# Kernel optimization log

Measured on AMD Instinct MI355X. Metric: run time of the kernel, lower is better.

Reference implementation:

```python
import jax, jax.numpy as jnp
import numpy as np

N = 50000
E = 800000
C_IN = 64
C_OUT = 64
K = 3  # Chebyshev order (num_stacks)
LAMBDA_MAX = 2.0


def setup_inputs() -> dict:
    key = jax.random.key(0)
    ks = jax.random.split(key, 32)
    inp = {
        'X': jax.random.normal(ks[0], (N, C_IN), dtype=jnp.float32),
        'edge_index': jax.random.randint(ks[1], (2, E), 0, N, dtype=jnp.int64),
        'edge_weight': jax.random.uniform(ks[2], (E,), dtype=jnp.float32),
        'H': jax.random.normal(ks[3], (N, C_OUT), dtype=jnp.float32),
        'C': jax.random.normal(ks[4], (N, C_OUT), dtype=jnp.float32),
    }
    # 8 ChebConvs: conv_{x,h}_{i,f,c,o}; x-convs map C_IN->C_OUT, h-convs C_OUT->C_OUT
    names_x = ['Wxi', 'Wxf', 'Wxc', 'Wxo']
    names_h = ['Whi', 'Whf', 'Whc', 'Who']
    i = 5
    for nx, nh in zip(names_x, names_h):
        inp[nx] = jax.random.normal(ks[i], (K, C_IN, C_OUT), dtype=jnp.float32) * (1.0 / np.sqrt(K * C_IN)); i += 1
        inp['b' + nx[1:]] = jax.random.normal(ks[i], (C_OUT,), dtype=jnp.float32) * 0.01; i += 1
        inp[nh] = jax.random.normal(ks[i], (K, C_OUT, C_OUT), dtype=jnp.float32) * (1.0 / np.sqrt(K * C_OUT)); i += 1
        inp['b' + nh[1:]] = jax.random.normal(ks[i], (C_OUT,), dtype=jnp.float32) * 0.01; i += 1
    # per-gate biases b_i, b_f, b_c, b_o of shape [1, C_OUT] (zero-initialized in torch)
    for nm in ['bi', 'bf', 'bc', 'bo']:
        inp[nm] = jax.random.normal(ks[i], (1, C_OUT), dtype=jnp.float32) * 0.01; i += 1
    return inp


def _cheb_norm(edge_index, edge_weight, n):
    # symmetric normalization: D^-1/2 W D^-1/2 (PyG get_laplacian 'sym')
    row, col = edge_index[0], edge_index[1]
    deg = jax.ops.segment_sum(edge_weight, row, num_segments=n)
    dinv = jnp.where(deg > 0, jax.lax.rsqrt(jnp.where(deg > 0, deg, 1.0)), 0.0)
    return dinv[row] * edge_weight * dinv[col]


def _cheb_conv(x, W, b, row, col, nw, n):
    # ChebConv: out = sum_k T_k(L_hat) x @ W[k] + b, with
    # L_hat v = (2/lambda_max) * (v - A_norm v) - v
    def Lhat(v):
        agg = jax.ops.segment_sum(nw[:, None] * v[col], row, num_segments=n)
        return (2.0 / LAMBDA_MAX) * (v - agg) - v
    Tx_prev = x
    out = x @ W[0]
    k = W.shape[0]
    if k > 1:
        Tx = Lhat(x)
        out = out + Tx @ W[1]
        for j in range(2, k):
            Tx_new = 2.0 * Lhat(Tx) - Tx_prev
            out = out + Tx_new @ W[j]
            Tx_prev, Tx = Tx, Tx_new
    return out + b


def reference(X, edge_index, edge_weight, H, C,
              Wxi, bxi, Whi, bhi, Wxf, bxf, Whf, bhf,
              Wxc, bxc, Whc, bhc, Wxo, bxo, Who, bho,
              bi, bf, bc, bo):
    n = X.shape[0]
    row, col = edge_index[0], edge_index[1]
    nw = _cheb_norm(edge_index, edge_weight, n)
    cc = lambda v, W, b: _cheb_conv(v, W, b, row, col, nw, n)
    I = jax.nn.sigmoid(cc(X, Wxi, bxi) + cc(H, Whi, bhi) + bi)
    F = jax.nn.sigmoid(cc(X, Wxf, bxf) + cc(H, Whf, bhf) + bf)
    T = jnp.tanh(cc(X, Wxc, bxc) + cc(H, Whc, bhc) + bc)
    C_new = F * C + I * T
    O = jax.nn.sigmoid(cc(X, Wxo, bxo) + cc(H, Who, bho) + bo)
    H_new = O * jnp.tanh(C_new)
    return (H_new, C_new)
```

## Files before the change

### kernel.cpp

```cpp
#include <hip/hip_runtime.h>

#define N_NODES 50000
#define N_PAD   50048
#define N_EDGES 800000
#define NBE4    782
#define NB_IL2  1563

typedef __attribute__((ext_vector_type(8))) short bf16x8;
typedef __attribute__((ext_vector_type(4))) float f32x4;

__device__ __forceinline__ unsigned short f2bf(float f) {
    unsigned u = __float_as_uint(f);
    u = (u + 0x7fffu + ((u >> 16) & 1u)) >> 16;
    return (unsigned short)u;
}

__device__ __forceinline__ float fsig(float x) {
    x = fminf(fmaxf(x, -30.f), 30.f);
    float t = __expf(x);
    return __fdividef(t, 1.f + t);
}
__device__ __forceinline__ float ftanh(float x) {
    x = fminf(fmaxf(x, -15.f), 15.f);
    float t = __expf(2.f * x);
    return 1.f - __fdividef(2.f, t + 1.f);
}


__global__ __launch_bounds__(256) void k_deg_prep(
    const void* __restrict__ eiraw, const float* __restrict__ w,
    unsigned* __restrict__ packed, unsigned* __restrict__ rank,
    const float* __restrict__ X, const float* __restrict__ H, unsigned short* __restrict__ XH,
    const float* __restrict__ Wxi, const float* __restrict__ Whi,
    const float* __restrict__ Wxf, const float* __restrict__ Whf,
    const float* __restrict__ Wxc, const float* __restrict__ Whc,
    const float* __restrict__ Wxo, const float* __restrict__ Who,
    const float* __restrict__ bxi, const float* __restrict__ bhi,
    const float* __restrict__ bxf, const float* __restrict__ bhf,
    const float* __restrict__ bxc, const float* __restrict__ bhc,
    const float* __restrict__ bxo, const float* __restrict__ bho,
    const float* __restrict__ bgi, const float* __restrict__ bgf,
    const float* __restrict__ bgc, const float* __restrict__ bgo,
    unsigned short* __restrict__ Wf, float* __restrict__ ball) {
    __shared__ int sflag;
    int b = blockIdx.x, t = threadIdx.x;
    if (b < NBE4) {
        if (t == 0) sflag = 0;
        __syncthreads();
        int si = b * 1024 + t;
        int sv = ((const int*)eiraw)[1 + 2 * si];
        if (sv) atomicOr(&sflag, 1);
        __syncthreads();
        int is32 = sflag;

        int rr[4]; unsigned qq[4]; int ee[4];
#pragma unroll
        for (int k = 0; k < 4; k++) {
            int e = b * 1024 + k * 256 + t;
            ee[k] = e;
            if (e < N_EDGES) {
                rr[k] = is32 ? ((const int*)eiraw)[e] : (int)(((const long long*)eiraw)[e]);
                qq[k] = (unsigned)(w[e] * 65536.f + 0.5f);
            } else {
                rr[k] = -1;
            }
        }
#pragma unroll
        for (int k = 0; k < 4; k++) {
            if (rr[k] >= 0) {
                unsigned old = atomicAdd(&packed[rr[k]], (1u << 22) | qq[k]);
                rank[ee[k]] = old >> 22;
            }
        }
        return;
    }
    int bb = b - NBE4;
    if (bb < NB_IL2) {
        int tt = bb * 256 + t;
        int node = tt >> 3, g = tt & 7;
        if (node >= N_NODES) return;
        const float* base = (g < 4) ? (X + (size_t)node * 64 + g * 16)
                                    : (H + (size_t)node * 64 + (g - 4) * 16);
        float4 v0 = ((const float4*)base)[0];
        float4 v1 = ((const float4*)base)[1];
        float4 v2 = ((const float4*)base)[2];
        float4 v3 = ((const float4*)base)[3];
        uint4 o0, o1;
        o0.x = (unsigned)f2bf(v0.x) | ((unsigned)f2bf(v0.y) << 16);
        o0.y = (unsigned)f2bf(v0.z) | ((unsigned)f2bf(v0.w) << 16);
        o0.z = (unsigned)f2bf(v1.x) | ((unsigned)f2bf(v1.y) << 16);
        o0.w = (unsigned)f2bf(v1.z) | ((unsigned)f2bf(v1.w) << 16);
        o1.x = (unsigned)f2bf(v2.x) | ((unsigned)f2bf(v2.y) << 16);
        o1.y = (unsigned)f2bf(v2.z) | ((unsigned)f2bf(v2.w) << 16);
        o1.z = (unsigned)f2bf(v3.x) | ((unsigned)f2bf(v3.y) << 16);
        o1.w = (unsigned)f2bf(v3.z) | ((unsigned)f2bf(v3.w) << 16);
        unsigned short* dst = XH + (size_t)node * 128 + g * 16;
        *(uint4*)dst = o0;
        *(uint4*)(dst + 8) = o1;
        return;
    }
    bb -= NB_IL2;
    if (bb < 48) {
        int flat = bb * 256 + t;
        int l = flat & 63, nt = (flat >> 6) & 15, ks = flat >> 10;
        int n = nt * 16 + (l & 15);
        int g = n >> 6, c = n & 63;
        const float* WX = (g == 0) ? Wxi : (g == 1) ? Wxf : (g == 2) ? Wxc : Wxo;
        const float* WH = (g == 0) ? Whi : (g == 1) ? Whf : (g == 2) ? Whc : Who;
        int k0 = ks * 32 + (l >> 4) * 8;
        unsigned short ov[8];
#pragma unroll
        for (int j = 0; j < 8; j++) {
            int k = k0 + j;
            int bsel = k >> 7, ch = k & 127;
            const float* W = (ch < 64) ? WX : WH;
            int kk = ch & 63;
            float v;
            if (bsel == 0)      v = W[kk * 64 + c] - W[2 * 4096 + kk * 64 + c];
            else if (bsel == 1) v = -W[4096 + kk * 64 + c];
            else                v = 2.f * W[2 * 4096 + kk * 64 + c];
            ov[j] = f2bf(v);
        }
        uint4 o;
        o.x = (unsigned)ov[0] | ((unsigned)ov[1] << 16);
        o.y = (unsigned)ov[2] | ((unsigned)ov[3] << 16);
        o.z = (unsigned)ov[4] | ((unsigned)ov[5] << 16);
        o.w = (unsigned)ov[6] | ((unsigned)ov[7] << 16);
        *(uint4*)(Wf + (size_t)flat * 8) = o;
    } else {
        int g = t >> 6, c = t & 63;
        const float* BX = (g == 0) ? bxi : (g == 1) ? bxf : (g == 2) ? bxc : bxo;
        const float* BH = (g == 0) ? bhi : (g == 1) ? bhf : (g == 2) ? bhc : bho;
        const float* BG = (g == 0) ? bgi : (g == 1) ? bgf : (g == 2) ? bgc : bgo;
        ball[t] = BX[c] + BH[c] + BG[c];
    }
}


__global__ __launch_bounds__(256) void k_scan1(const unsigned* __restrict__ packed,
                                               int* __restrict__ rp, int* __restrict__ part,
                                               float* __restrict__ dinv) {
    __shared__ int s[256];
    int t = threadIdx.x, i = blockIdx.x * 256 + t;
    unsigned p = (i < N_NODES) ? packed[i] : 0u;
    int v = (int)(p >> 22);
    s[t] = v; __syncthreads();
    for (int d = 1; d < 256; d <<= 1) {
        int add = (t >= d) ? s[t - d] : 0;
        __syncthreads();
        s[t] += add;
        __syncthreads();
    }
    if (i < N_NODES) {
        rp[i] = s[t] - v;
        float dg = (float)(p & 0x3fffffu) * (1.f / 65536.f);
        dinv[i] = (dg > 0.f) ? rsqrtf(dg) : 0.f;
        if (i == N_NODES - 1) rp[N_NODES] = s[t];
    }
    if (t == 255) part[blockIdx.x] = s[255];
}

__global__ __launch_bounds__(256) void k_scan2(int* __restrict__ part, int nb) {
    __shared__ int s[256];
    int t = threadIdx.x;
    int v = (t < nb) ? part[t] : 0;
    s[t] = v; __syncthreads();
    for (int d = 1; d < 256; d <<= 1) {
        int add = (t >= d) ? s[t - d] : 0;
        __syncthreads();
        s[t] += add;
        __syncthreads();
    }
    if (t < nb) part[t] = s[t] - v;
}

__global__ __launch_bounds__(256) void k_scatter(const void* __restrict__ eiraw, const float* __restrict__ w,
                                                 const unsigned* __restrict__ rank,
                                                 const float* __restrict__ dinv, const int* __restrict__ rp,
                                                 const int* __restrict__ part,
                                                 int* __restrict__ colp, float* __restrict__ nwp) {
    __shared__ int sflag;
    int b = blockIdx.x, t = threadIdx.x;
    if (t == 0) sflag = 0;
    __syncthreads();
    int si = b * 1024 + t;
    int sv = ((const int*)eiraw)[1 + 2 * si];
    if (sv) atomicOr(&sflag, 1);
    __syncthreads();
    int is32 = sflag;
#pragma unroll
    for (int k = 0; k < 4; k++) {
        int e = b * 1024 + k * 256 + t;
        if (e >= N_EDGES) break;
        int r, c;
        if (is32) { r = ((const int*)eiraw)[e]; c = ((const int*)eiraw)[N_EDGES + e]; }
        else      { r = (int)(((const long long*)eiraw)[e]); c = (int)(((const long long*)eiraw)[N_EDGES + e]); }
        int pos = rp[r] + part[r >> 8] + (int)rank[e];
        colp[pos] = c;
        nwp[pos] = dinv[r] * w[e] * dinv[c];
    }
}


__global__ __launch_bounds__(256) void k_spmv_bf(const unsigned short* __restrict__ src,
                                                 unsigned short* __restrict__ dst,
                                                 const int* __restrict__ rp, const int* __restrict__ part,
                                                 const int* __restrict__ colp, const float* __restrict__ nwp) {
    int wid = threadIdx.x >> 6, lane = threadIdx.x & 63;
    int node = blockIdx.x * 4 + wid;
    if (node >= N_NODES) return;
    int s = rp[node] + part[node >> 8];
    int e = rp[node + 1] + part[(node + 1) >> 8];
    float a0 = 0.f, a1 = 0.f;
    for (int jb = s; jb < e; jb += 8) {
        int   c[8]; float wv[8]; unsigned vv[8];
#pragma unroll
        for (int k = 0; k < 8; k++) {
            int j = jb + k;
            int jc = (j < e) ? j : (e - 1);
            c[k]  = colp[jc];
            wv[k] = (j < e) ? nwp[jc] : 0.f;
        }
#pragma unroll
        for (int k = 0; k < 8; k++)
            vv[k] = *(const unsigned*)(src + (size_t)c[k] * 128 + lane * 2);
#pragma unroll
        for (int k = 0; k < 8; k++) {
            a0 = fmaf(wv[k], __uint_as_float(vv[k] << 16), a0);
            a1 = fmaf(wv[k], __uint_as_float(vv[k] & 0xffff0000u), a1);
        }
    }
    unsigned o = (unsigned)f2bf(a0) | ((unsigned)f2bf(a1) << 16);
    *(unsigned*)(dst + (size_t)node * 128 + lane * 2) = o;
}


__global__ __launch_bounds__(256) void k_gemm_mfma(
    const unsigned short* __restrict__ XH, const unsigned short* __restrict__ U1,
    const unsigned short* __restrict__ U2, const unsigned short* __restrict__ Wf,
    const float* __restrict__ ball, const float* __restrict__ C, float* __restrict__ out) {
    __shared__ __align__(16) uint4 Bs[2][1024];

    int t = threadIdx.x;
    int wid = t >> 6, lane = t & 63;
    int col = lane & 15, quad = lane >> 4;
    int m0 = blockIdx.x * 64 + wid * 16;
    int arow = m0 + col;

    f32x4 acc[16];
#pragma unroll
    for (int i = 0; i < 16; i++) acc[i] = (f32x4){0.f, 0.f, 0.f, 0.f};

    const unsigned short* srcs[3] = {XH, U1, U2};

    bf16x8 a_cur = *(const bf16x8*)(srcs[0] + (size_t)arow * 128 + quad * 8);
    const uint4* g0 = (const uint4*)Wf;
    uint4 p0 = g0[t], p1 = g0[t + 256], p2 = g0[t + 512], p3 = g0[t + 768];

    for (int ks = 0; ks < 12; ks++) {
        uint4* dstb = Bs[ks & 1];
        dstb[t] = p0; dstb[t + 256] = p1; dstb[t + 512] = p2; dstb[t + 768] = p3;
        __syncthreads();
        bf16x8 a_nxt = a_cur;
        if (ks < 11) {
            int ks1 = ks + 1;
            const uint4* g = (const uint4*)(Wf + (size_t)ks1 * 8192);
            p0 = g[t]; p1 = g[t + 256]; p2 = g[t + 512]; p3 = g[t + 768];
            a_nxt = *(const bf16x8*)(srcs[ks1 >> 2] + (size_t)arow * 128 + (ks1 & 3) * 32 + quad * 8);
        }
        const unsigned short* B = (const unsigned short*)Bs[ks & 1];
#pragma unroll
        for (int nt = 0; nt < 16; nt++) {
            bf16x8 bfrag = *(const bf16x8*)(B + nt * 512 + lane * 8);
            acc[nt] = __builtin_amdgcn_mfma_f32_16x16x32_bf16(a_cur, bfrag, acc[nt], 0, 0, 0);
        }
        a_cur = a_nxt;
    }

    float bI[4], bF[4], bT[4], bO[4];
#pragma unroll
    for (int cq = 0; cq < 4; cq++) {
        int c = cq * 16 + col;
        bI[cq] = ball[c]; bF[cq] = ball[64 + c]; bT[cq] = ball[128 + c]; bO[cq] = ball[192 + c];
    }
#pragma unroll
    for (int r = 0; r < 4; r++) {
        int node = m0 + quad * 4 + r;
        if (node >= N_NODES) continue;
#pragma unroll
        for (int cq = 0; cq < 4; cq++) {
            int c = cq * 16 + col;
            float ig = fsig(acc[0 + cq][r]  + bI[cq]);
            float fg = fsig(acc[4 + cq][r]  + bF[cq]);
            float tg = ftanh(acc[8 + cq][r] + bT[cq]);
            float og = fsig(acc[12 + cq][r] + bO[cq]);
            float cv = fmaf(fg, C[(size_t)node * 64 + c], ig * tg);
            out[(size_t)node * 64 + c] = og * ftanh(cv);
            out[(size_t)N_NODES * 64 + (size_t)node * 64 + c] = cv;
        }
    }
}


extern "C" void kernel_launch(void* const* d_in, const int* in_sizes, int n_in,
                              void* d_out, int out_size, void* d_ws, size_t ws_size,
                              hipStream_t stream) {
    const float* X   = (const float*)d_in[0];
    const void*  ei  = d_in[1];
    const float* w   = (const float*)d_in[2];
    const float* H   = (const float*)d_in[3];
    const float* C   = (const float*)d_in[4];
    const float* Wxi = (const float*)d_in[5];  const float* bxi = (const float*)d_in[6];
    const float* Whi = (const float*)d_in[7];  const float* bhi = (const float*)d_in[8];
    const float* Wxf = (const float*)d_in[9];  const float* bxf = (const float*)d_in[10];
    const float* Whf = (const float*)d_in[11]; const float* bhf = (const float*)d_in[12];
    const float* Wxc = (const float*)d_in[13]; const float* bxc = (const float*)d_in[14];
    const float* Whc = (const float*)d_in[15]; const float* bhc = (const float*)d_in[16];
    const float* Wxo = (const float*)d_in[17]; const float* bxo = (const float*)d_in[18];
    const float* Who = (const float*)d_in[19]; const float* bho = (const float*)d_in[20];
    const float* bgi = (const float*)d_in[21]; const float* bgf = (const float*)d_in[22];
    const float* bgc = (const float*)d_in[23]; const float* bgo = (const float*)d_in[24];
    float* out = (float*)d_out;

    char* ws = (char*)d_ws;
    size_t off = 0;
    auto alloc = [&](size_t bytes) -> char* {
        char* p = ws + off;
        off = (off + bytes + 255) & ~(size_t)255;
        return p;
    };
    unsigned* packed = (unsigned*)alloc((size_t)N_NODES * 4);
    unsigned* rank = (unsigned*)alloc((size_t)N_EDGES * 4);
    int*   rp   = (int*)alloc((N_NODES + 1) * 4);
    int*   part = (int*)alloc(256 * 4);
    float* dinv = (float*)alloc(N_NODES * 4);
    int*   colp = (int*)alloc((size_t)(N_EDGES + 8) * 4);
    float* nwp  = (float*)alloc((size_t)(N_EDGES + 8) * 4);
    unsigned short* XH = (unsigned short*)alloc((size_t)N_PAD * 128 * 2);
    unsigned short* U1 = (unsigned short*)alloc((size_t)N_PAD * 128 * 2);
    unsigned short* U2 = (unsigned short*)alloc((size_t)N_PAD * 128 * 2);
    unsigned short* Wf = (unsigned short*)alloc((size_t)12 * 16 * 64 * 8 * 2);
    float* ball = (float*)alloc(256 * 4);
    (void)ws_size; (void)in_sizes; (void)n_in; (void)out_size;

    hipMemsetAsync(packed, 0, (size_t)N_NODES * 4, stream);

    int nbN = (N_NODES + 255) / 256;

    k_deg_prep<<<NBE4 + NB_IL2 + 49, 256, 0, stream>>>(ei, w, packed, rank, X, H, XH,
                                                       Wxi, Whi, Wxf, Whf, Wxc, Whc, Wxo, Who,
                                                       bxi, bhi, bxf, bhf, bxc, bhc, bxo, bho,
                                                       bgi, bgf, bgc, bgo, Wf, ball);
    k_scan1<<<nbN, 256, 0, stream>>>(packed, rp, part, dinv);
    k_scan2<<<1, 256, 0, stream>>>(part, nbN);
    k_scatter<<<NBE4, 256, 0, stream>>>(ei, w, rank, dinv, rp, part, colp, nwp);
    k_spmv_bf<<<(N_NODES + 3) / 4, 256, 0, stream>>>(XH, U1, rp, part, colp, nwp);
    k_spmv_bf<<<(N_NODES + 3) / 4, 256, 0, stream>>>(U1, U2, rp, part, colp, nwp);
    k_gemm_mfma<<<(N_NODES + 63) / 64, 256, 0, stream>>>(XH, U1, U2, Wf, ball, C, out);
}
```

Before: 302.0 us.

## Build CSR via two-level bucket sort instead of per-node global atomics

Replaces the global per-node atomic degree/rank counting with a bucketed counting sort: per-block shared-memory histograms over 256-node buckets, a scan of the histogram, a scatter of packed edges into buckets, and a per-bucket LDS build of CSR rows and degrees. The edge normalization is moved into the first SpMV, which also writes the normalized weights for the second SpMV. This targets global atomic contention and the extra rank array traffic, at the cost of more kernels, an 8-byte edge buffer, and a 16-bit column packing that relies on N < 65536. Buckets larger than the LDS capacity fall back to re-reading global memory.

```diff
diff --git a/kernel.cpp b/kernel.cpp
--- a/kernel.cpp
+++ b/kernel.cpp
@@ -5,6 +5,8 @@
 #define N_EDGES 800000
 #define NBE4    782
 #define NB_IL2  1563
+#define NBKT    196
+#define BCAP    4992
 
 typedef __attribute__((ext_vector_type(8))) short bf16x8;
 typedef __attribute__((ext_vector_type(4))) float f32x4;
@@ -27,9 +29,9 @@
 }
 
 
-__global__ __launch_bounds__(256) void k_deg_prep(
-    const void* __restrict__ eiraw, const float* __restrict__ w,
-    unsigned* __restrict__ packed, unsigned* __restrict__ rank,
+__global__ __launch_bounds__(256) void k_prep(
+    const void* __restrict__ eiraw,
+    unsigned* __restrict__ hist,
     const float* __restrict__ X, const float* __restrict__ H, unsigned short* __restrict__ XH,
     const float* __restrict__ Wxi, const float* __restrict__ Whi,
     const float* __restrict__ Wxf, const float* __restrict__ Whf,
@@ -43,35 +45,27 @@
     const float* __restrict__ bgc, const float* __restrict__ bgo,
     unsigned short* __restrict__ Wf, float* __restrict__ ball) {
     __shared__ int sflag;
+    __shared__ unsigned cnt[NBKT];
     int b = blockIdx.x, t = threadIdx.x;
     if (b < NBE4) {
         if (t == 0) sflag = 0;
+        if (t < NBKT) cnt[t] = 0;
         __syncthreads();
         int si = b * 1024 + t;
         int sv = ((const int*)eiraw)[1 + 2 * si];
         if (sv) atomicOr(&sflag, 1);
         __syncthreads();
         int is32 = sflag;
-
-        int rr[4]; unsigned qq[4]; int ee[4];
 #pragma unroll
         for (int k = 0; k < 4; k++) {
             int e = b * 1024 + k * 256 + t;
-            ee[k] = e;
             if (e < N_EDGES) {
-                rr[k] = is32 ? ((const int*)eiraw)[e] : (int)(((const long long*)eiraw)[e]);
-                qq[k] = (unsigned)(w[e] * 65536.f + 0.5f);
-            } else {
-                rr[k] = -1;
+                int r = is32 ? ((const int*)eiraw)[e] : (int)(((const long long*)eiraw)[e]);
+                atomicAdd(&cnt[r >> 8], 1u);
             }
         }
-#pragma unroll
-        for (int k = 0; k < 4; k++) {
-            if (rr[k] >= 0) {
-                unsigned old = atomicAdd(&packed[rr[k]], (1u << 22) | qq[k]);
-                rank[ee[k]] = old >> 22;
-            }
-        }
+        __syncthreads();
+        if (t < NBKT) hist[(size_t)t * NBE4 + b] = cnt[t];
         return;
     }
     int bb = b - NBE4;
@@ -137,51 +131,60 @@
 }
 
 
-__global__ __launch_bounds__(256) void k_scan1(const unsigned* __restrict__ packed,
-                                               int* __restrict__ rp, int* __restrict__ part,
-                                               float* __restrict__ dinv) {
-    __shared__ int s[256];
-    int t = threadIdx.x, i = blockIdx.x * 256 + t;
-    unsigned p = (i < N_NODES) ? packed[i] : 0u;
-    int v = (int)(p >> 22);
+__global__ __launch_bounds__(256) void k_bscan(unsigned* __restrict__ hist, unsigned* __restrict__ btot) {
+    __shared__ unsigned s[256];
+    int j = blockIdx.x, t = threadIdx.x;
+    unsigned* row = hist + (size_t)j * NBE4;
+    unsigned v[4];
+#pragma unroll
+    for (int k = 0; k < 4; k++) {
+        int i = t * 4 + k;
+        v[k] = (i < NBE4) ? row[i] : 0u;
+    }
+    unsigned tsum = v[0] + v[1] + v[2] + v[3];
+    s[t] = tsum; __syncthreads();
+    for (int d = 1; d < 256; d <<= 1) {
+        unsigned a = (t >= d) ? s[t - d] : 0u;
+        __syncthreads();
+        s[t] += a;
+        __syncthreads();
+    }
+    unsigned run = s[t] - tsum;
+#pragma unroll
+    for (int k = 0; k < 4; k++) {
+        int i = t * 4 + k;
+        if (i < NBE4) { unsigned c = v[k]; row[i] = run; run += c; }
+    }
+    if (t == 255) btot[j] = s[255];
+}
+
+
+__global__ __launch_bounds__(256) void k_btot(const unsigned* __restrict__ btot,
+                                              unsigned* __restrict__ bbase, int* __restrict__ rp) {
+    __shared__ unsigned s[256];
+    int t = threadIdx.x;
+    unsigned v = (t < NBKT) ? btot[t] : 0u;
     s[t] = v; __syncthreads();
     for (int d = 1; d < 256; d <<= 1) {
-        int add = (t >= d) ? s[t - d] : 0;
-        __syncthreads();
-        s[t] += add;
-        __syncthreads();
-    }
-    if (i < N_NODES) {
-        rp[i] = s[t] - v;
-        float dg = (float)(p & 0x3fffffu) * (1.f / 65536.f);
-        dinv[i] = (dg > 0.f) ? rsqrtf(dg) : 0.f;
-        if (i == N_NODES - 1) rp[N_NODES] = s[t];
-    }
-    if (t == 255) part[blockIdx.x] = s[255];
-}
-
-__global__ __launch_bounds__(256) void k_scan2(int* __restrict__ part, int nb) {
-    __shared__ int s[256];
-    int t = threadIdx.x;
-    int v = (t < nb) ? part[t] : 0;
-    s[t] = v; __syncthreads();
-    for (int d = 1; d < 256; d <<= 1) {
-        int add = (t >= d) ? s[t - d] : 0;
-        __syncthreads();
-        s[t] += add;
-        __syncthreads();
-    }
-    if (t < nb) part[t] = s[t] - v;
-}
-
-__global__ __launch_bounds__(256) void k_scatter(const void* __restrict__ eiraw, const float* __restrict__ w,
-                                                 const unsigned* __restrict__ rank,
-                                                 const float* __restrict__ dinv, const int* __restrict__ rp,
-                                                 const int* __restrict__ part,
-                                                 int* __restrict__ colp, float* __restrict__ nwp) {
+        unsigned a = (t >= d) ? s[t - d] : 0u;
+        __syncthreads();
+        s[t] += a;
+        __syncthreads();
+    }
+    if (t < NBKT) bbase[t] = s[t] - v;
+    if (t == 0) { bbase[NBKT] = N_EDGES; rp[N_NODES] = N_EDGES; }
+}
+
+
+__global__ __launch_bounds__(256) void k_scat(const void* __restrict__ eiraw, const float* __restrict__ w,
+                                              const unsigned* __restrict__ hist, const unsigned* __restrict__ bbase,
+                                              unsigned long long* __restrict__ ebuf) {
     __shared__ int sflag;
+    __shared__ unsigned boff[NBKT];
+    __shared__ unsigned cur[NBKT];
     int b = blockIdx.x, t = threadIdx.x;
     if (t == 0) sflag = 0;
+    if (t < NBKT) { boff[t] = bbase[t] + hist[(size_t)t * NBE4 + b]; cur[t] = 0u; }
     __syncthreads();
     int si = b * 1024 + t;
     int sv = ((const int*)eiraw)[1 + 2 * si];
@@ -191,26 +194,118 @@
 #pragma unroll
     for (int k = 0; k < 4; k++) {
         int e = b * 1024 + k * 256 + t;
-        if (e >= N_EDGES) break;
-        int r, c;
-        if (is32) { r = ((const int*)eiraw)[e]; c = ((const int*)eiraw)[N_EDGES + e]; }
-        else      { r = (int)(((const long long*)eiraw)[e]); c = (int)(((const long long*)eiraw)[N_EDGES + e]); }
-        int pos = rp[r] + part[r >> 8] + (int)rank[e];
-        colp[pos] = c;
-        nwp[pos] = dinv[r] * w[e] * dinv[c];
-    }
-}
-
+        if (e < N_EDGES) {
+            int r, c;
+            if (is32) { r = ((const int*)eiraw)[e]; c = ((const int*)eiraw)[N_EDGES + e]; }
+            else      { r = (int)(((const long long*)eiraw)[e]); c = (int)(((const long long*)eiraw)[N_EDGES + e]); }
+            float wv = w[e];
+            int bk = r >> 8;
+            unsigned lr = atomicAdd(&cur[bk], 1u);
+            unsigned pos = boff[bk] + lr;
+            ebuf[pos] = ((unsigned long long)(unsigned)r << 48)
+                      | (((unsigned long long)(unsigned)c & 0xffffull) << 32)
+                      | (unsigned long long)__float_as_uint(wv);
+        }
+    }
+}
+
+
+__global__ __launch_bounds__(1024) void k_build(const unsigned long long* __restrict__ ebuf,
+                                                const unsigned* __restrict__ bbase,
+                                                int* __restrict__ rp, float* __restrict__ dinv,
+                                                int* __restrict__ colp, float* __restrict__ wraw) {
+    __shared__ unsigned long long se[BCAP];
+    __shared__ unsigned cnt[256];
+    __shared__ float wsum[256];
+    __shared__ unsigned off[256];
+    __shared__ unsigned cur[256];
+    int b = blockIdx.x, t = threadIdx.x;
+    unsigned base = bbase[b], end = bbase[b + 1];
+    int n = (int)(end - base);
+    if (t < 256) { cnt[t] = 0u; wsum[t] = 0.f; }
+    __syncthreads();
+    for (int i = t; i < n; i += 1024) {
+        unsigned long long e = ebuf[base + i];
+        if (i < BCAP) se[i] = e;
+        unsigned lr = (unsigned)(e >> 48) & 255u;
+        atomicAdd(&cnt[lr], 1u);
+        atomicAdd(&wsum[lr], __uint_as_float((unsigned)(e & 0xffffffffu)));
+    }
+    __syncthreads();
+    if (t < 256) off[t] = cnt[t];
+    __syncthreads();
+    for (int d = 1; d < 256; d <<= 1) {
+        unsigned a = 0u;
+        if (t < 256 && t >= d) a = off[t - d];
+        __syncthreads();
+        if (t < 256) off[t] += a;
+        __syncthreads();
+    }
+    if (t < 256) {
+        unsigned excl = off[t] - cnt[t];
+        off[t] = excl;
+        cur[t] = excl;
+        int row = b * 256 + t;
+        if (row < N_NODES) {
+            rp[row] = (int)(base + excl);
+            float dg = wsum[t];
+            dinv[row] = (dg > 0.f) ? rsqrtf(dg) : 0.f;
+        }
+    }
+    __syncthreads();
+    for (int i = t; i < n; i += 1024) {
+        unsigned long long e = (i < BCAP) ? se[i] : ebuf[base + i];
+        unsigned lr = (unsigned)(e >> 48) & 255u;
+        unsigned p = atomicAdd(&cur[lr], 1u);
+        colp[base + p] = (int)((e >> 32) & 0xffffu);
+        wraw[base + p] = __uint_as_float((unsigned)(e & 0xffffffffu));
+    }
+}
+
+
+__global__ __launch_bounds__(256) void k_spmv_nw(const unsigned short* __restrict__ src,
+                                                 unsigned short* __restrict__ dst,
+                                                 const int* __restrict__ rp, const int* __restrict__ colp,
+                                                 const float* __restrict__ wraw, const float* __restrict__ dinv,
+                                                 float* __restrict__ nwp) {
+    int wid = threadIdx.x >> 6, lane = threadIdx.x & 63;
+    int node = blockIdx.x * 4 + wid;
+    if (node >= N_NODES) return;
+    int s = rp[node], e = rp[node + 1];
+    float dr = dinv[node];
+    float a0 = 0.f, a1 = 0.f;
+    for (int jb = s; jb < e; jb += 8) {
+        int   c[8]; float wv[8]; unsigned vv[8];
+#pragma unroll
+        for (int k = 0; k < 8; k++) {
+            int j = jb + k;
+            int jc = (j < e) ? j : (e - 1);
+            c[k]  = colp[jc];
+            float nw = dr * wraw[jc] * dinv[c[k]];
+            wv[k] = (j < e) ? nw : 0.f;
+            if (lane == 0 && j < e) nwp[jc] = nw;
+        }
+#pragma unroll
+        for (int k = 0; k < 8; k++)
+            vv[k] = *(const unsigned*)(src + (size_t)c[k] * 128 + lane * 2);
+#pragma unroll
+        for (int k = 0; k < 8; k++) {
+            a0 = fmaf(wv[k], __uint_as_float(vv[k] << 16), a0);
+            a1 = fmaf(wv[k], __uint_as_float(vv[k] & 0xffff0000u), a1);
+        }
+    }
+    unsigned o = (unsigned)f2bf(a0) | ((unsigned)f2bf(a1) << 16);
+    *(unsigned*)(dst + (size_t)node * 128 + lane * 2) = o;
+}
 
 __global__ __launch_bounds__(256) void k_spmv_bf(const unsigned short* __restrict__ src,
                                                  unsigned short* __restrict__ dst,
-                                                 const int* __restrict__ rp, const int* __restrict__ part,
+                                                 const int* __restrict__ rp,
                                                  const int* __restrict__ colp, const float* __restrict__ nwp) {
     int wid = threadIdx.x >> 6, lane = threadIdx.x & 63;
     int node = blockIdx.x * 4 + wid;
     if (node >= N_NODES) return;
-    int s = rp[node] + part[node >> 8];
-    int e = rp[node + 1] + part[(node + 1) >> 8];
+    int s = rp[node], e = rp[node + 1];
     float a0 = 0.f, a1 = 0.f;
     for (int jb = s; jb < e; jb += 8) {
         int   c[8]; float wv[8]; unsigned vv[8];
@@ -329,12 +424,14 @@
         off = (off + bytes + 255) & ~(size_t)255;
         return p;
     };
-    unsigned* packed = (unsigned*)alloc((size_t)N_NODES * 4);
-    unsigned* rank = (unsigned*)alloc((size_t)N_EDGES * 4);
+    unsigned* hist  = (unsigned*)alloc((size_t)NBKT * NBE4 * 4);
+    unsigned* btot  = (unsigned*)alloc((NBKT + 1) * 4);
+    unsigned* bbase = (unsigned*)alloc((NBKT + 1) * 4);
+    unsigned long long* ebuf = (unsigned long long*)alloc((size_t)N_EDGES * 8);
     int*   rp   = (int*)alloc((N_NODES + 1) * 4);
-    int*   part = (int*)alloc(256 * 4);
     float* dinv = (float*)alloc(N_NODES * 4);
     int*   colp = (int*)alloc((size_t)(N_EDGES + 8) * 4);
+    float* wraw = (float*)alloc((size_t)(N_EDGES + 8) * 4);
     float* nwp  = (float*)alloc((size_t)(N_EDGES + 8) * 4);
     unsigned short* XH = (unsigned short*)alloc((size_t)N_PAD * 128 * 2);
     unsigned short* U1 = (unsigned short*)alloc((size_t)N_PAD * 128 * 2);
@@ -343,18 +440,15 @@
     float* ball = (float*)alloc(256 * 4);
     (void)ws_size; (void)in_sizes; (void)n_in; (void)out_size;
 
-    hipMemsetAsync(packed, 0, (size_t)N_NODES * 4, stream);
-
-    int nbN = (N_NODES + 255) / 256;
-
-    k_deg_prep<<<NBE4 + NB_IL2 + 49, 256, 0, stream>>>(ei, w, packed, rank, X, H, XH,
-                                                       Wxi, Whi, Wxf, Whf, Wxc, Whc, Wxo, Who,
-                                                       bxi, bhi, bxf, bhf, bxc, bhc, bxo, bho,
-                                                       bgi, bgf, bgc, bgo, Wf, ball);
-    k_scan1<<<nbN, 256, 0, stream>>>(packed, rp, part, dinv);
-    k_scan2<<<1, 256, 0, stream>>>(part, nbN);
-    k_scatter<<<NBE4, 256, 0, stream>>>(ei, w, rank, dinv, rp, part, colp, nwp);
-    k_spmv_bf<<<(N_NODES + 3) / 4, 256, 0, stream>>>(XH, U1, rp, part, colp, nwp);
-    k_spmv_bf<<<(N_NODES + 3) / 4, 256, 0, stream>>>(U1, U2, rp, part, colp, nwp);
+    k_prep<<<NBE4 + NB_IL2 + 49, 256, 0, stream>>>(ei, hist, X, H, XH,
+                                                   Wxi, Whi, Wxf, Whf, Wxc, Whc, Wxo, Who,
+                                                   bxi, bhi, bxf, bhf, bxc, bhc, bxo, bho,
+                                                   bgi, bgf, bgc, bgo, Wf, ball);
+    k_bscan<<<NBKT, 256, 0, stream>>>(hist, btot);
+    k_btot<<<1, 256, 0, stream>>>(btot, bbase, rp);
+    k_scat<<<NBE4, 256, 0, stream>>>(ei, w, hist, bbase, ebuf);
+    k_build<<<NBKT, 1024, 0, stream>>>(ebuf, bbase, rp, dinv, colp, wraw);
+    k_spmv_nw<<<(N_NODES + 3) / 4, 256, 0, stream>>>(XH, U1, rp, colp, wraw, dinv, nwp);
+    k_spmv_bf<<<(N_NODES + 3) / 4, 256, 0, stream>>>(U1, U2, rp, colp, nwp);
     k_gemm_mfma<<<(N_NODES + 63) / 64, 256, 0, stream>>>(XH, U1, U2, Wf, ball, C, out);
 }
```

Result: slower. 313.2 us (+3.7%).
